# Performance work log

Measured on AMD Instinct MI355X. Metric: run time of the kernel, lower is better.

The kernel has to match this reference:

```python
import jax, jax.numpy as jnp
from jax import lax
import numpy as np

D_MODEL, D_STATE, D_CONV, EXPAND = 192, 16, 3, 2
D_INNER = EXPAND * D_MODEL
B_, H_, W_ = 8, 128, 128
PAD = (D_CONV - 1) // 2
EPS = 1e-5


def setup_inputs() -> dict:
    key = jax.random.key(0)
    ks = jax.random.split(key, 8)
    s = 0.02
    return {
        "x": jax.random.normal(ks[0], (B_, D_MODEL, H_, W_), jnp.float32),
        "w_in": jax.random.normal(ks[1], (D_MODEL, 2 * D_INNER), jnp.float32) * s,
        "w_conv": jax.random.normal(ks[2], (D_INNER, 1, D_CONV, D_CONV), jnp.float32) * s,
        "b_conv": jnp.zeros((D_INNER,), jnp.float32),
        "w_x": jax.random.normal(ks[3], (D_INNER, 2 * D_STATE), jnp.float32) * s,
        "w_dt": jax.random.normal(ks[4], (D_STATE, D_INNER), jnp.float32) * s,
        "b_dt": jnp.zeros((D_INNER,), jnp.float32),
        "D_skip": jnp.ones((D_INNER,), jnp.float32),
        "w_out": jax.random.normal(ks[5], (D_INNER, D_MODEL), jnp.float32) * s,
        "gamma": jnp.ones((D_INNER,), jnp.float32),
        "beta": jnp.zeros((D_INNER,), jnp.float32),
    }


def _ss2d(x, w_in, w_conv, b_conv, w_x, w_dt, b_dt, D_skip, w_out, gamma, beta):
    B, C, H, W = x.shape
    L = H * W
    # NOTE: faithful to torch: x.reshape(B, H*W, C) on an NCHW tensor is a raw
    # row-major reinterpretation (same semantics as jnp.reshape), not a transpose.
    x_flat = x.reshape(B, L, C)
    x_proj = x_flat @ w_in                     # [B, L, 2*d_inner]
    x_inner, z = jnp.split(x_proj, 2, axis=-1)
    # depthwise conv over spatial dims
    xc = jnp.transpose(x_inner, (0, 2, 1)).reshape(B, D_INNER, H, W)
    xc = lax.conv_general_dilated(
        xc, w_conv, window_strides=(1, 1), padding=[(PAD, PAD), (PAD, PAD)],
        dimension_numbers=("NCHW", "OIHW", "NCHW"), feature_group_count=D_INNER,
    ) + b_conv[None, :, None, None]
    xc = jax.nn.silu(xc)
    xc = jnp.transpose(xc.reshape(B, D_INNER, L), (0, 2, 1))   # [B, L, d_inner]
    x_ssm = xc @ w_x                                            # [B, L, 2*d_state]
    B_ssm, C_ssm = jnp.split(x_ssm, 2, axis=-1)
    dt = jax.nn.softplus(B_ssm @ w_dt + b_dt)                   # [B, L, d_inner]
    # Original: deltaB = dt[...,None]*B_ssm[:,:,None,:]; einsum('blid,bld->bli', deltaB, C_ssm)
    # == dt * sum_d(B_ssm*C_ssm)  (deltaA is computed but never used -> dropped)
    bc = jnp.sum(B_ssm * C_ssm, axis=-1, keepdims=True)         # [B, L, 1]
    y = dt * bc + xc * D_skip                                   # [B, L, d_inner]
    y = y * jax.nn.silu(z)
    mu = jnp.mean(y, axis=-1, keepdims=True)
    var = jnp.mean(jnp.square(y - mu), axis=-1, keepdims=True)
    y = (y - mu) * lax.rsqrt(var + EPS) * gamma + beta
    out = y @ w_out                                             # [B, L, d_model]
    return jnp.transpose(out, (0, 2, 1)).reshape(B, C, H, W)


def reference(x, w_in, w_conv, b_conv, w_x, w_dt, b_dt, D_skip, w_out, gamma, beta):
    return _ss2d(x, w_in, w_conv, b_conv, w_x, w_dt, b_dt, D_skip, w_out, gamma, beta)
```

## Files before the change

### kernel.cpp

```cpp
#include <hip/hip_runtime.h>
#include <hip/hip_bf16.h>

typedef __bf16 bf16x8 __attribute__((ext_vector_type(8)));
typedef __bf16 bf16x4 __attribute__((ext_vector_type(4)));
typedef float  f32x4  __attribute__((ext_vector_type(4)));

__device__ __forceinline__ f32x4 mfma16(bf16x8 a, bf16x8 b, f32x4 c) {
    return __builtin_amdgcn_mfma_f32_16x16x32_bf16(a, b, c, 0, 0, 0);
}
__device__ __forceinline__ float silu_f(float v) { return v / (1.f + __expf(-v)); }
__device__ __forceinline__ float softplus_fast(float v) {
    float r = __logf(1.f + __expf(v));
    return v > 15.f ? v : r;
}

#define CC 192
#define DI 384
#define LL 16384
#define HH 128
#define WW 128

__global__ void k0_prep(const float* __restrict__ w_in, const float* __restrict__ w_x,
                        const float* __restrict__ w_dt, const float* __restrict__ w_out,
                        __bf16* __restrict__ wt_in, __bf16* __restrict__ wt_x,
                        __bf16* __restrict__ wt_dt, __bf16* __restrict__ wt_out) {
    int tid = blockIdx.x * blockDim.x + threadIdx.x;
    int nth = gridDim.x * blockDim.x;
    for (int i = tid; i < 768 * 192; i += nth) {
        int nf = i / 192, k = i % 192;
        int nc = nf >> 6, n = nf & 63;
        int e = (n * 192 + k) ^ ((n & 7) << 3);
        wt_in[nc * 12288 + e] = (__bf16)w_in[k * 768 + nf];
    }
    for (int i = tid; i < 32 * 384;  i += nth) { int n = i / 384, k = i % 384; wt_x[i]  = (__bf16)w_x[k * 32 + n]; }
    for (int i = tid; i < 384 * 16;  i += nth) { int ch = i / 16, k = i % 16;  wt_dt[i] = (__bf16)w_dt[k * 384 + ch]; }
    for (int i = tid; i < 192 * 384; i += nth) { int n = i / 384, k = i % 384; wt_out[i] = (__bf16)w_out[k * 192 + n]; }
}

__global__ __launch_bounds__(256, 2) void k1_proj(
        const float* __restrict__ x, const __bf16* __restrict__ wt_in,
        __bf16* __restrict__ xin, __bf16* __restrict__ zsb) {
    __shared__ __attribute__((aligned(16))) __bf16 Bs[2][12288];
    __shared__ __attribute__((aligned(16))) __bf16 bounce[4][32 * 68];
    const int tid = threadIdx.x;
    const int lane = tid & 63, wv = tid >> 6;
    const int lq = lane & 15, quad = lane >> 4;
    const long mbase = (long)blockIdx.x * 128;
    __bf16* bb = &bounce[wv][0];

    bf16x8 af[2][6];
#pragma unroll
    for (int mt = 0; mt < 2; mt++) {
        const float* xr = x + (mbase + wv * 32 + mt * 16 + lq) * CC;
#pragma unroll
        for (int ks = 0; ks < 6; ks++) {
            float4 v0 = *(const float4*)(xr + ks * 32 + quad * 8);
            float4 v1 = *(const float4*)(xr + ks * 32 + quad * 8 + 4);
            bf16x8 t;
            t[0] = (__bf16)v0.x; t[1] = (__bf16)v0.y; t[2] = (__bf16)v0.z; t[3] = (__bf16)v0.w;
            t[4] = (__bf16)v1.x; t[5] = (__bf16)v1.y; t[6] = (__bf16)v1.z; t[7] = (__bf16)v1.w;
            af[mt][ks] = t;
        }
    }

    auto stage = [&](int b, int nc) {
        const char* src = (const char*)(wt_in + nc * 12288);
        char* dst = (char*)&Bs[b][0];
#pragma unroll
        for (int i = 0; i < 6; i++) {
            int off = (wv * 6 + i) * 1024;
            __builtin_amdgcn_global_load_lds(
                (const __attribute__((address_space(1))) void*)(src + off + lane * 16),
                (__attribute__((address_space(3))) void*)(dst + off),
                16, 0, 0);
        }
    };

    stage(0, 0);
    __syncthreads();

    int buf = 0;
    for (int nc = 0; nc < 12; nc++) {
        if (nc < 11) stage(buf ^ 1, nc + 1);

        f32x4 A0[4], A1[4];
#pragma unroll
        for (int nt = 0; nt < 4; nt++) {
            A0[nt] = (f32x4){0.f, 0.f, 0.f, 0.f};
            A1[nt] = (f32x4){0.f, 0.f, 0.f, 0.f};
#pragma unroll
            for (int ks = 0; ks < 6; ks++) {
                const int row = nt * 16 + lq;
                const int e = (row * 192 + ks * 32 + quad * 8) ^ ((lq & 7) << 3);
                bf16x8 bf = *(const bf16x8*)(&Bs[buf][e]);
                A0[nt] = mfma16(af[0][ks], bf, A0[nt]);
                A1[nt] = mfma16(af[1][ks], bf, A1[nt]);
            }
        }
        const bool isz = (nc >= 6);
#pragma unroll
        for (int nt = 0; nt < 4; nt++) {
#pragma unroll
            for (int r = 0; r < 4; r++) {
                float v0 = A0[nt][r], v1 = A1[nt][r];
                if (isz) { v0 = silu_f(v0); v1 = silu_f(v1); }
                bb[(quad * 4 + r) * 68 + nt * 16 + lq] = (__bf16)v0;
                bb[(16 + quad * 4 + r) * 68 + nt * 16 + lq] = (__bf16)v1;
            }
        }
        __builtin_amdgcn_wave_barrier();
        __bf16* dst = isz ? zsb : xin;
        const int chb = (isz ? nc - 6 : nc) * 64;
#pragma unroll
        for (int k = 0; k < 4; k++) {
            int u = lane + k * 64;
            int row = u >> 3, c8 = u & 7;
            unsigned long long lo = *(const unsigned long long*)(&bb[row * 68 + c8 * 8]);
            unsigned long long hi = *(const unsigned long long*)(&bb[row * 68 + c8 * 8 + 4]);
            ulonglong2 val; val.x = lo; val.y = hi;
            *(ulonglong2*)(dst + (mbase + wv * 32 + row) * DI + chb + c8 * 8) = val;
        }
        __syncthreads();
        buf ^= 1;
    }
}

__global__ __launch_bounds__(512, 2) void k3_ssm(
        const __bf16* __restrict__ xin, const __bf16* __restrict__ zsb,
        const __bf16* __restrict__ wtx, const __bf16* __restrict__ wtdt,
        const __bf16* __restrict__ wtout, const float* __restrict__ wconv,
        const float* __restrict__ bconv, const float* __restrict__ bdt,
        const float* __restrict__ dskip, const float* __restrict__ gamma,
        const float* __restrict__ beta, float* __restrict__ out) {
    __shared__ __attribute__((aligned(16))) float smem0[13056];
    __shared__ __attribute__((aligned(16))) __bf16 dts[64 * 200];
    __shared__ float bcarr[64];
    __bf16* xcb = (__bf16*)smem0;
    float* otile = smem0;

    const int tid = threadIdx.x;
    const int lane = tid & 63, wv = tid >> 6;
    const int lq = lane & 15, quad = lane >> 4;
    const int t0g = blockIdx.x * 64;

    const int te = tid >> 3, part = tid & 7;
    const long tok = t0g + te;

    bf16x8 zpre[6];
#pragma unroll
    for (int h = 0; h < 2; h++)
#pragma unroll
        for (int g = 0; g < 3; g++)
            zpre[h * 3 + g] = *(const bf16x8*)(zsb + tok * DI + h * 192 + part * 24 + g * 8);

    float* wcvs = (float*)dts;
    float* bcvs = wcvs + 9 * 384;
    for (int u = tid; u < 9 * 384; u += 512) { int ch = u / 9, tap = u % 9; wcvs[tap * 384 + ch] = wconv[u]; }
    for (int u = tid; u < 384; u += 512) bcvs[u] = bconv[u];
    __syncthreads();

    const int hblk = (t0g & (LL - 1)) >> 7;
    const int w0 = t0g & 127;
#pragma unroll
    for (int k = 0; k < 6; k++) {
        int u = tid + k * 512;
        int t = u / 48, c8 = u % 48;
        long tk = t0g + t;
        float acc[8];
        float4 b0 = *(const float4*)(bcvs + c8 * 8);
        float4 b1 = *(const float4*)(bcvs + c8 * 8 + 4);
        acc[0] = b0.x; acc[1] = b0.y; acc[2] = b0.z; acc[3] = b0.w;
        acc[4] = b1.x; acc[5] = b1.y; acc[6] = b1.z; acc[7] = b1.w;
#pragma unroll
        for (int dy = -1; dy <= 1; dy++) {
            int h2 = hblk + dy;
            if (h2 < 0 || h2 >= HH) continue;
#pragma unroll
            for (int dx = -1; dx <= 1; dx++) {
                int w2 = w0 + t + dx;
                if (w2 < 0 || w2 >= WW) continue;
                bf16x8 v = *(const bf16x8*)(xin + (tk + dy * WW + dx) * (long)DI + c8 * 8);
                const float* wp = &wcvs[((dy + 1) * 3 + (dx + 1)) * 384 + c8 * 8];
#pragma unroll
                for (int j = 0; j < 8; j++) acc[j] += (float)v[j] * wp[j];
            }
        }
        bf16x8 r;
#pragma unroll
        for (int j = 0; j < 8; j++) r[j] = (__bf16)silu_f(acc[j]);
        *(bf16x8*)(&xcb[t * 392 + c8 * 8]) = r;
    }
    __syncthreads();

    float* Bf = (float*)dts;
    float* Cf = Bf + 64 * 20;
    {
        const int wt = wv & 3, wsel = wv >> 2;
        f32x4 a4 = {0.f, 0.f, 0.f, 0.f};
#pragma unroll
        for (int ks = 0; ks < 12; ks++) {
            bf16x8 a = *(const bf16x8*)(&xcb[(wt * 16 + lq) * 392 + ks * 32 + quad * 8]);
            bf16x8 b = *(const bf16x8*)(wtx + (wsel * 16 + lq) * 384 + ks * 32 + quad * 8);
            a4 = mfma16(a, b, a4);
        }
        float* dstf = wsel ? Cf : Bf;
#pragma unroll
        for (int r = 0; r < 4; r++)
            dstf[(wt * 16 + quad * 4 + r) * 20 + lq] = a4[r];
    }
    __syncthreads();

    {
        int t = tid >> 3;
        int s0 = (tid & 7) * 2;
        float p = Bf[t * 20 + s0] * Cf[t * 20 + s0] + Bf[t * 20 + s0 + 1] * Cf[t * 20 + s0 + 1];
        p += __shfl_xor(p, 1, 64);
        p += __shfl_xor(p, 2, 64);
        p += __shfl_xor(p, 4, 64);
        if ((lane & 7) == 0) bcarr[t] = p;
    }
    bf16x8 zero8;
#pragma unroll
    for (int j = 0; j < 8; j++) zero8[j] = (__bf16)0.f;
    bf16x8 aA[4];
#pragma unroll
    for (int mt = 0; mt < 4; mt++) {
        if (quad < 2) {
            const float* bp = Bf + (mt * 16 + lq) * 20 + quad * 8;
            f32x4 lo = *(const f32x4*)(bp);
            f32x4 hi = *(const f32x4*)(bp + 4);
            bf16x8 t8;
            t8[0] = (__bf16)lo[0]; t8[1] = (__bf16)lo[1]; t8[2] = (__bf16)lo[2]; t8[3] = (__bf16)lo[3];
            t8[4] = (__bf16)hi[0]; t8[5] = (__bf16)hi[1]; t8[6] = (__bf16)hi[2]; t8[7] = (__bf16)hi[3];
            aA[mt] = t8;
        } else {
            aA[mt] = zero8;
        }
    }
    __syncthreads();

    float s1 = 0.f, s2 = 0.f;

#pragma unroll
    for (int h = 0; h < 2; h++) {
        f32x4 dacc[2][4];
        float bdtv[2];
#pragma unroll
        for (int j = 0; j < 2; j++) {
            const int tile = wv + 8 * j;
            if (tile < 12) {
                int chg = h * 192 + tile * 16 + lq;
                bf16x8 bf = (quad < 2) ? *(const bf16x8*)(wtdt + (long)chg * 16 + quad * 8) : zero8;
                bdtv[j] = bdt[chg];
#pragma unroll
                for (int mt = 0; mt < 4; mt++) {
                    f32x4 z4 = {0.f, 0.f, 0.f, 0.f};
                    dacc[j][mt] = mfma16(aA[mt], bf, z4);
                }
            }
        }
#pragma unroll
        for (int j = 0; j < 2; j++) {
            const int tile = wv + 8 * j;
            if (tile < 12) {
#pragma unroll
                for (int mt = 0; mt < 4; mt++)
#pragma unroll
                    for (int r = 0; r < 4; r++)
                        dts[(mt * 16 + quad * 4 + r) * 200 + tile * 16 + lq] =
                            (__bf16)(dacc[j][mt][r] + bdtv[j]);
            }
        }
        __syncthreads();

#pragma unroll
        for (int g = 0; g < 3; g++) {
            const int chl = part * 24 + g * 8;
            const int chg = h * 192 + chl;
            bf16x8 d8 = *(const bf16x8*)(&dts[te * 200 + chl]);
            bf16x8 xc8 = *(const bf16x8*)(&xcb[te * 392 + chg]);
            bf16x8 z8 = zpre[h * 3 + g];
            float4 d0 = *(const float4*)(dskip + chg);
            float4 d1 = *(const float4*)(dskip + chg + 4);
            float ds[8] = {d0.x, d0.y, d0.z, d0.w, d1.x, d1.y, d1.z, d1.w};
            const float bcv = bcarr[te];
#pragma unroll
            for (int j = 0; j < 8; j++) {
                float dtv = softplus_fast((float)d8[j]);
                float yv = (dtv * bcv + (float)xc8[j] * ds[j]) * (float)z8[j];
                s1 += yv; s2 += yv * yv;
                xc8[j] = (__bf16)yv;
            }
            *(bf16x8*)(&xcb[te * 392 + chg]) = xc8;
        }
        __syncthreads();
    }

    {
        s1 += __shfl_xor(s1, 1, 64); s2 += __shfl_xor(s2, 1, 64);
        s1 += __shfl_xor(s1, 2, 64); s2 += __shfl_xor(s2, 2, 64);
        s1 += __shfl_xor(s1, 4, 64); s2 += __shfl_xor(s2, 4, 64);
        float mu = s1 * (1.f / 384.f);
        float var = s2 * (1.f / 384.f) - mu * mu;
        float rstd = rsqrtf(var + 1e-5f);
#pragma unroll
        for (int gg = 0; gg < 6; gg++) {
            const int h2 = gg / 3, g3 = gg % 3;
            const int ch = h2 * 192 + part * 24 + g3 * 8;
            bf16x8 v = *(const bf16x8*)(&xcb[te * 392 + ch]);
            float4 g0 = *(const float4*)(gamma + ch);
            float4 g1 = *(const float4*)(gamma + ch + 4);
            float4 be0 = *(const float4*)(beta + ch);
            float4 be1 = *(const float4*)(beta + ch + 4);
            float gm[8] = {g0.x, g0.y, g0.z, g0.w, g1.x, g1.y, g1.z, g1.w};
            float bt[8] = {be0.x, be0.y, be0.z, be0.w, be1.x, be1.y, be1.z, be1.w};
#pragma unroll
            for (int j = 0; j < 8; j++) v[j] = (__bf16)(((float)v[j] - mu) * rstd * gm[j] + bt[j]);
            *(bf16x8*)(&xcb[te * 392 + ch]) = v;
        }
    }
    __syncthreads();

    {
        const int mh = wv >> 2, nb = (wv & 3) * 3;
        f32x4 acc[3][2];
#pragma unroll
        for (int j = 0; j < 3; j++)
#pragma unroll
            for (int m2 = 0; m2 < 2; m2++) acc[j][m2] = (f32x4){0.f, 0.f, 0.f, 0.f};
#pragma unroll
        for (int ks = 0; ks < 12; ks++) {
            bf16x8 bfr[3];
#pragma unroll
            for (int j = 0; j < 3; j++) {
                int c = (nb + j) * 16 + lq;
                bfr[j] = *(const bf16x8*)(wtout + (long)c * 384 + ks * 32 + quad * 8);
            }
#pragma unroll
            for (int m2 = 0; m2 < 2; m2++) {
                bf16x8 afr = *(const bf16x8*)(&xcb[((mh * 2 + m2) * 16 + lq) * 392 + ks * 32 + quad * 8]);
#pragma unroll
                for (int j = 0; j < 3; j++) acc[j][m2] = mfma16(afr, bfr[j], acc[j][m2]);
            }
        }
        __syncthreads();
#pragma unroll
        for (int j = 0; j < 3; j++) {
            int c = (nb + j) * 16 + lq;
#pragma unroll
            for (int m2 = 0; m2 < 2; m2++)
#pragma unroll
                for (int r = 0; r < 4; r++)
                    otile[c * 68 + (mh * 2 + m2) * 16 + quad * 4 + r] = acc[j][m2][r];
        }
    }
    __syncthreads();

    {
        const int bimg = t0g >> 14;
        const int l0 = t0g & (LL - 1);
#pragma unroll
        for (int k = 0; k < 6; k++) {
            int u = tid + k * 512;
            int c = u >> 4, j = u & 15;
            float4 v = *(const float4*)(&otile[c * 68 + j * 4]);
            *(float4*)(out + ((long)(bimg * CC + c)) * LL + l0 + j * 4) = v;
        }
    }
}

extern "C" void kernel_launch(void* const* d_in, const int* in_sizes, int n_in,
                              void* d_out, int out_size, void* d_ws, size_t ws_size,
                              hipStream_t stream) {
    (void)in_sizes; (void)n_in; (void)out_size; (void)ws_size;
    const float* x      = (const float*)d_in[0];
    const float* w_in   = (const float*)d_in[1];
    const float* w_conv = (const float*)d_in[2];
    const float* b_conv = (const float*)d_in[3];
    const float* w_x    = (const float*)d_in[4];
    const float* w_dt   = (const float*)d_in[5];
    const float* b_dt   = (const float*)d_in[6];
    const float* D_skip = (const float*)d_in[7];
    const float* w_out  = (const float*)d_in[8];
    const float* gamma  = (const float*)d_in[9];
    const float* beta   = (const float*)d_in[10];
    float* out = (float*)d_out;

    char* ws = (char*)d_ws;
    __bf16* wt_in  = (__bf16*)(ws);
    __bf16* wt_x   = (__bf16*)(ws + 294912);
    __bf16* wt_dt  = (__bf16*)(ws + 319488);
    __bf16* wt_out = (__bf16*)(ws + 331776);
    __bf16* xin    = (__bf16*)(ws + 479232);
    __bf16* zsb    = (__bf16*)(ws + 479232 + 100663296);

    k0_prep<<<96, 256, 0, stream>>>(w_in, w_x, w_dt, w_out, wt_in, wt_x, wt_dt, wt_out);
    k1_proj<<<1024, 256, 0, stream>>>(x, wt_in, xin, zsb);
    k3_ssm<<<2048, 512, 0, stream>>>(xin, zsb, wt_x, wt_dt, wt_out, w_conv, b_conv,
                                     b_dt, D_skip, gamma, beta, out);
}
```

Before: 550.3 us.

## Chunk intermediate layout by 64 channels and halve SSM block tile to 32 tokens

```diff
diff --git a/kernel.cpp b/kernel.cpp
--- a/kernel.cpp
+++ b/kernel.cpp
@@ -19,6 +19,8 @@
 #define LL 16384
 #define HH 128
 #define WW 128
+#define LTOT 131072L
+
 
 __global__ void k0_prep(const float* __restrict__ w_in, const float* __restrict__ w_x,
                         const float* __restrict__ w_dt, const float* __restrict__ w_out,
@@ -110,7 +112,7 @@
         }
         __builtin_amdgcn_wave_barrier();
         __bf16* dst = isz ? zsb : xin;
-        const int chb = (isz ? nc - 6 : nc) * 64;
+        const long chunk = isz ? nc - 6 : nc;
 #pragma unroll
         for (int k = 0; k < 4; k++) {
             int u = lane + k * 64;
@@ -118,30 +120,33 @@
             unsigned long long lo = *(const unsigned long long*)(&bb[row * 68 + c8 * 8]);
             unsigned long long hi = *(const unsigned long long*)(&bb[row * 68 + c8 * 8 + 4]);
             ulonglong2 val; val.x = lo; val.y = hi;
-            *(ulonglong2*)(dst + (mbase + wv * 32 + row) * DI + chb + c8 * 8) = val;
+            *(ulonglong2*)(dst + (chunk * LTOT + mbase + wv * 32 + row) * 64 + c8 * 8) = val;
         }
         __syncthreads();
         buf ^= 1;
     }
 }
 
-__global__ __launch_bounds__(512, 2) void k3_ssm(
+__global__ __launch_bounds__(256, 4) void k3_ssm(
         const __bf16* __restrict__ xin, const __bf16* __restrict__ zsb,
         const __bf16* __restrict__ wtx, const __bf16* __restrict__ wtdt,
         const __bf16* __restrict__ wtout, const float* __restrict__ wconv,
         const float* __restrict__ bconv, const float* __restrict__ bdt,
         const float* __restrict__ dskip, const float* __restrict__ gamma,
         const float* __restrict__ beta, float* __restrict__ out) {
-    __shared__ __attribute__((aligned(16))) float smem0[13056];
-    __shared__ __attribute__((aligned(16))) __bf16 dts[64 * 200];
-    __shared__ float bcarr[64];
-    __bf16* xcb = (__bf16*)smem0;
-    float* otile = smem0;
+    __shared__ __attribute__((aligned(16))) __bf16 xcb[32 * 392];
+    __shared__ __attribute__((aligned(16))) char region1[15360];
+    float* wcvs = (float*)region1;
+    float* bcvs = (float*)(region1 + 13824);
+    float* Bf   = (float*)region1;
+    float* Cf   = (float*)(region1 + 2560);
+    __bf16* dts = (__bf16*)region1;
+    float* bcarr = (float*)(region1 + 12800);
 
     const int tid = threadIdx.x;
     const int lane = tid & 63, wv = tid >> 6;
     const int lq = lane & 15, quad = lane >> 4;
-    const int t0g = blockIdx.x * 64;
+    const int t0g = blockIdx.x * 32;
 
     const int te = tid >> 3, part = tid & 7;
     const long tok = t0g + te;
@@ -150,22 +155,24 @@
 #pragma unroll
     for (int h = 0; h < 2; h++)
 #pragma unroll
-        for (int g = 0; g < 3; g++)
-            zpre[h * 3 + g] = *(const bf16x8*)(zsb + tok * DI + h * 192 + part * 24 + g * 8);
-
-    float* wcvs = (float*)dts;
-    float* bcvs = wcvs + 9 * 384;
-    for (int u = tid; u < 9 * 384; u += 512) { int ch = u / 9, tap = u % 9; wcvs[tap * 384 + ch] = wconv[u]; }
-    for (int u = tid; u < 384; u += 512) bcvs[u] = bconv[u];
+        for (int g = 0; g < 3; g++) {
+            const int chg = h * 192 + part * 24 + g * 8;
+            zpre[h * 3 + g] = *(const bf16x8*)(zsb + ((long)(chg >> 6) * LTOT + tok) * 64 + (chg & 63));
+        }
+
+    for (int u = tid; u < 9 * 384; u += 256) { int ch = u / 9, tap = u % 9; wcvs[tap * 384 + ch] = wconv[u]; }
+    for (int u = tid; u < 384; u += 256) bcvs[u] = bconv[u];
     __syncthreads();
 
     const int hblk = (t0g & (LL - 1)) >> 7;
     const int w0 = t0g & 127;
 #pragma unroll
     for (int k = 0; k < 6; k++) {
-        int u = tid + k * 512;
+        int u = tid + k * 256;
         int t = u / 48, c8 = u % 48;
         long tk = t0g + t;
+        const long cbase = (long)(c8 >> 3) * LTOT;
+        const int coff = (c8 & 7) * 8;
         float acc[8];
         float4 b0 = *(const float4*)(bcvs + c8 * 8);
         float4 b1 = *(const float4*)(bcvs + c8 * 8 + 4);
@@ -179,7 +186,7 @@
             for (int dx = -1; dx <= 1; dx++) {
                 int w2 = w0 + t + dx;
                 if (w2 < 0 || w2 >= WW) continue;
-                bf16x8 v = *(const bf16x8*)(xin + (tk + dy * WW + dx) * (long)DI + c8 * 8);
+                bf16x8 v = *(const bf16x8*)(xin + (cbase + tk + dy * WW + dx) * 64 + coff);
                 const float* wp = &wcvs[((dy + 1) * 3 + (dx + 1)) * 384 + c8 * 8];
 #pragma unroll
                 for (int j = 0; j < 8; j++) acc[j] += (float)v[j] * wp[j];
@@ -192,10 +199,8 @@
     }
     __syncthreads();
 
-    float* Bf = (float*)dts;
-    float* Cf = Bf + 64 * 20;
     {
-        const int wt = wv & 3, wsel = wv >> 2;
+        const int wt = wv & 1, wsel = wv >> 1;
         f32x4 a4 = {0.f, 0.f, 0.f, 0.f};
 #pragma unroll
         for (int ks = 0; ks < 12; ks++) {
@@ -222,9 +227,9 @@
     bf16x8 zero8;
 #pragma unroll
     for (int j = 0; j < 8; j++) zero8[j] = (__bf16)0.f;
-    bf16x8 aA[4];
-#pragma unroll
-    for (int mt = 0; mt < 4; mt++) {
+    bf16x8 aA[2];
+#pragma unroll
+    for (int mt = 0; mt < 2; mt++) {
         if (quad < 2) {
             const float* bp = Bf + (mt * 16 + lq) * 20 + quad * 8;
             f32x4 lo = *(const f32x4*)(bp);
@@ -243,34 +248,27 @@
 
 #pragma unroll
     for (int h = 0; h < 2; h++) {
-        f32x4 dacc[2][4];
-        float bdtv[2];
-#pragma unroll
-        for (int j = 0; j < 2; j++) {
-            const int tile = wv + 8 * j;
-            if (tile < 12) {
-                int chg = h * 192 + tile * 16 + lq;
-                bf16x8 bf = (quad < 2) ? *(const bf16x8*)(wtdt + (long)chg * 16 + quad * 8) : zero8;
-                bdtv[j] = bdt[chg];
-#pragma unroll
-                for (int mt = 0; mt < 4; mt++) {
-                    f32x4 z4 = {0.f, 0.f, 0.f, 0.f};
-                    dacc[j][mt] = mfma16(aA[mt], bf, z4);
-                }
-            }
-        }
-#pragma unroll
-        for (int j = 0; j < 2; j++) {
-            const int tile = wv + 8 * j;
-            if (tile < 12) {
-#pragma unroll
-                for (int mt = 0; mt < 4; mt++)
-#pragma unroll
-                    for (int r = 0; r < 4; r++)
-                        dts[(mt * 16 + quad * 4 + r) * 200 + tile * 16 + lq] =
-                            (__bf16)(dacc[j][mt][r] + bdtv[j]);
-            }
-        }
+        f32x4 dacc[3][2];
+        float bdtv[3];
+#pragma unroll
+        for (int j = 0; j < 3; j++) {
+            int chg = h * 192 + (wv * 3 + j) * 16 + lq;
+            bf16x8 bf = (quad < 2) ? *(const bf16x8*)(wtdt + (long)chg * 16 + quad * 8) : zero8;
+            bdtv[j] = bdt[chg];
+#pragma unroll
+            for (int mt = 0; mt < 2; mt++) {
+                f32x4 z4 = {0.f, 0.f, 0.f, 0.f};
+                dacc[j][mt] = mfma16(aA[mt], bf, z4);
+            }
+        }
+#pragma unroll
+        for (int j = 0; j < 3; j++)
+#pragma unroll
+            for (int mt = 0; mt < 2; mt++)
+#pragma unroll
+                for (int r = 0; r < 4; r++)
+                    dts[(mt * 16 + quad * 4 + r) * 200 + (wv * 3 + j) * 16 + lq] =
+                        (__bf16)(dacc[j][mt][r] + bdtv[j]);
         __syncthreads();
 
 #pragma unroll
@@ -322,49 +320,34 @@
     __syncthreads();
 
     {
-        const int mh = wv >> 2, nb = (wv & 3) * 3;
+        const int bimg = t0g >> 14;
+        const int l0 = t0g & (LL - 1);
         f32x4 acc[3][2];
 #pragma unroll
         for (int j = 0; j < 3; j++)
 #pragma unroll
-            for (int m2 = 0; m2 < 2; m2++) acc[j][m2] = (f32x4){0.f, 0.f, 0.f, 0.f};
+            for (int mt = 0; mt < 2; mt++) acc[j][mt] = (f32x4){0.f, 0.f, 0.f, 0.f};
 #pragma unroll
         for (int ks = 0; ks < 12; ks++) {
             bf16x8 bfr[3];
 #pragma unroll
             for (int j = 0; j < 3; j++) {
-                int c = (nb + j) * 16 + lq;
+                int c = (wv * 3 + j) * 16 + lq;
                 bfr[j] = *(const bf16x8*)(wtout + (long)c * 384 + ks * 32 + quad * 8);
             }
 #pragma unroll
-            for (int m2 = 0; m2 < 2; m2++) {
-                bf16x8 afr = *(const bf16x8*)(&xcb[((mh * 2 + m2) * 16 + lq) * 392 + ks * 32 + quad * 8]);
-#pragma unroll
-                for (int j = 0; j < 3; j++) acc[j][m2] = mfma16(afr, bfr[j], acc[j][m2]);
-            }
-        }
-        __syncthreads();
+            for (int mt = 0; mt < 2; mt++) {
+                bf16x8 afr = *(const bf16x8*)(&xcb[(mt * 16 + lq) * 392 + ks * 32 + quad * 8]);
+#pragma unroll
+                for (int j = 0; j < 3; j++) acc[j][mt] = mfma16(afr, bfr[j], acc[j][mt]);
+            }
+        }
 #pragma unroll
         for (int j = 0; j < 3; j++) {
-            int c = (nb + j) * 16 + lq;
-#pragma unroll
-            for (int m2 = 0; m2 < 2; m2++)
-#pragma unroll
-                for (int r = 0; r < 4; r++)
-                    otile[c * 68 + (mh * 2 + m2) * 16 + quad * 4 + r] = acc[j][m2][r];
-        }
-    }
-    __syncthreads();
-
-    {
-        const int bimg = t0g >> 14;
-        const int l0 = t0g & (LL - 1);
-#pragma unroll
-        for (int k = 0; k < 6; k++) {
-            int u = tid + k * 512;
-            int c = u >> 4, j = u & 15;
-            float4 v = *(const float4*)(&otile[c * 68 + j * 4]);
-            *(float4*)(out + ((long)(bimg * CC + c)) * LL + l0 + j * 4) = v;
+            const int c = (wv * 3 + j) * 16 + lq;
+#pragma unroll
+            for (int mt = 0; mt < 2; mt++)
+                *(f32x4*)(out + ((long)(bimg * CC + c)) * LL + l0 + mt * 16 + quad * 4) = acc[j][mt];
         }
     }
 }
@@ -396,6 +379,6 @@
 
     k0_prep<<<96, 256, 0, stream>>>(w_in, w_x, w_dt, w_out, wt_in, wt_x, wt_dt, wt_out);
     k1_proj<<<1024, 256, 0, stream>>>(x, wt_in, xin, zsb);
-    k3_ssm<<<2048, 512, 0, stream>>>(xin, zsb, wt_x, wt_dt, wt_out, w_conv, b_conv,
+    k3_ssm<<<4096, 256, 0, stream>>>(xin, zsb, wt_x, wt_dt, wt_out, w_conv, b_conv,
                                      b_dt, D_skip, gamma, beta, out);
 }
```

Measured after the change: 468.3 us. 14.9% less time.
